# Optimization experiments

Hardware: AMD Instinct MI355X
Metric: run time of the kernel (lower is better)

Reference implementation:

```python
import jax, jax.numpy as jnp
import numpy as np

HIDDEN = 300
INPUT_DIM = 300


def setup_inputs() -> dict:
    key = jax.random.key(0)
    k_in, k_wih, k_whh, k_bih, k_bhh = jax.random.split(key, 5)
    bound = 1.0 / np.sqrt(HIDDEN)  # PyTorch RNNCell init: U(-1/sqrt(H), 1/sqrt(H))
    inputs = jax.random.normal(k_in, (512, 512, INPUT_DIM), dtype=jnp.float32)
    W_ih = jax.random.uniform(k_wih, (HIDDEN, INPUT_DIM), jnp.float32, -bound, bound)
    W_hh = jax.random.uniform(k_whh, (HIDDEN, HIDDEN), jnp.float32, -bound, bound)
    b_ih = jax.random.uniform(k_bih, (HIDDEN,), jnp.float32, -bound, bound)
    b_hh = jax.random.uniform(k_bhh, (HIDDEN,), jnp.float32, -bound, bound)
    return {"inputs": inputs, "W_ih": W_ih, "W_hh": W_hh, "b_ih": b_ih, "b_hh": b_hh}


def reference(inputs, W_ih, W_hh, b_ih, b_hh):
    # inputs: [seq, batch, input_dim]; vanilla tanh RNNCell scanned over time.
    seq, bz, _ = inputs.shape
    # Precompute input projections for all timesteps in one big GEMM.
    x_proj = jnp.einsum('sbi,hi->sbh', inputs, W_ih) + b_ih + b_hh  # [seq, batch, H]

    def step(ht, xp):
        ht = jnp.tanh(xp + ht @ W_hh.T)
        return ht, None

    h0 = jnp.zeros((bz, HIDDEN), dtype=inputs.dtype)
    ht, _ = jax.lax.scan(step, h0, x_proj)
    return ht
```

## Files before the change

### kernel.cpp

```cpp
#include <hip/hip_runtime.h>
#include <hip/hip_bf16.h>


typedef unsigned short u16;
typedef unsigned int   u32;
typedef __attribute__((ext_vector_type(8)))  short bf16x8;
typedef __attribute__((ext_vector_type(4)))  short s16x4;
typedef __attribute__((ext_vector_type(4)))  float f32x4;
typedef __attribute__((ext_vector_type(16))) float f32x16;
typedef __attribute__((ext_vector_type(2)))  unsigned int u32x2;
typedef __attribute__((ext_vector_type(4)))  unsigned int u32x4;

#define HID 300
#define KP  320
#define SEQ 512
#define BZ  512
#define MTOT (SEQ*BZ)

__device__ __forceinline__ u16 f2bf(float f) {
    u32 u = __float_as_uint(f);
    return (u16)((u + 0x7FFFu + ((u >> 16) & 1u)) >> 16);
}
__device__ __forceinline__ float bf2f(u16 h) {
    return __uint_as_float((u32)h << 16);
}
__device__ __forceinline__ float tanh_fast(float x) {
    float e = __builtin_amdgcn_exp2f(x * 2.8853900817779268f);
    float r = __builtin_amdgcn_rcpf(e + 1.0f);
    return __builtin_fmaf(-2.0f, r, 1.0f);
}
__device__ __forceinline__ u32 pack2(float a, float b) {
    __hip_bfloat162 t = __float22bfloat162_rn(float2{a, b});
    return *(u32*)&t;
}
__device__ __forceinline__ void lds_barrier() {
    asm volatile("s_waitcnt lgkmcnt(0)\n\ts_barrier" ::: "memory");
}

__global__ void prep_kernel(const float* __restrict__ wih,
                            const float* __restrict__ whh,
                            const float* __restrict__ bih,
                            const float* __restrict__ bhh,
                            u16* __restrict__ wihp, u16* __restrict__ whhp,
                            float* __restrict__ bias) {
    int n = blockIdx.x, k = threadIdx.x;
    bool v = (n < HID) && (k < HID);
    int src = n * HID + k, dst = n * KP + k;
    wihp[dst] = v ? f2bf(wih[src]) : (u16)0;
    whhp[dst] = v ? f2bf(whh[src]) : (u16)0;
    if (k == 0) bias[n] = (n < HID) ? (bih[n] + bhh[n]) : 0.0f;
}

__global__ __launch_bounds__(512, 1) void xproj_kernel(
    const float* __restrict__ in, const u16* __restrict__ wihp,
    const float* __restrict__ bias, u16* __restrict__ xp) {
    __shared__ __align__(16) u16 As[2][4096];
    __shared__ __align__(16) u16 Bs[2][10240];

    const int tid = threadIdx.x;
    const int w = tid >> 6, l = tid & 63;
    const int mi = w & 3, ni = w >> 2;
    const int l31 = l & 31, l5 = l >> 5;
    const int m0 = blockIdx.x * 128;

    const int sm = tid >> 2, skg = tid & 3;

    f32x16 acc[5];
#pragma unroll
    for (int j = 0; j < 5; ++j)
#pragma unroll
        for (int r = 0; r < 16; ++r) acc[j][r] = 0.0f;

    auto loadA = [&](int it, f32x4& v0, f32x4& v1) {
        int gk = it * 32 + skg * 8;
        const float* p = in + (size_t)(m0 + sm) * HID + gk;
        if (gk <= 292) { v0 = *(const f32x4*)p; v1 = *(const f32x4*)(p + 4); }
        else if (gk <= 296) { v0 = *(const f32x4*)p; v1 = f32x4{0.f,0.f,0.f,0.f}; }
        else { v0 = f32x4{0.f,0.f,0.f,0.f}; v1 = f32x4{0.f,0.f,0.f,0.f}; }
    };
    auto writeA = [&](int buf, const f32x4& v0, const f32x4& v1) {
        u32x4 pk;
        pk[0] = pack2(v0[0], v0[1]); pk[1] = pack2(v0[2], v0[3]);
        pk[2] = pack2(v1[0], v1[1]); pk[3] = pack2(v1[2], v1[3]);
        *(u32x4*)&As[buf][(skg >> 1) * 2048 + sm * 16 + (skg & 1) * 8] = pk;
    };
    auto stageB = [&](int buf, int it) {
#pragma unroll
        for (int s = 0; s < 3; ++s) {
            int i = w + 8 * s;
            if (i < 20) {
                int c = i & 3, ng = i >> 2;
                int n = ng * 64 + l;
                const u16* g = wihp + n * KP + it * 32 + c * 8;
                u16* d = &Bs[buf][c * 2560 + ng * 512];
                __builtin_amdgcn_global_load_lds(
                    (const __attribute__((address_space(1))) void*)g,
                    (__attribute__((address_space(3))) void*)d, 16, 0, 0);
            }
        }
    };

    {
        f32x4 v0, v1;
        loadA(0, v0, v1);
        writeA(0, v0, v1);
        stageB(0, 0);
    }
    __syncthreads();

#pragma unroll 1
    for (int it = 0; it < 10; ++it) {
        const int cb = it & 1, nb = (it + 1) & 1;
        f32x4 v0, v1;
        if (it < 9) {
            loadA(it + 1, v0, v1);
            stageB(nb, it + 1);
        }
#pragma unroll
        for (int s = 0; s < 2; ++s) {
            bf16x8 a = *(const bf16x8*)&As[cb][s * 2048 + mi * 512 + l31 * 16 + l5 * 8];
#pragma unroll
            for (int j = 0; j < 5; ++j) {
                bf16x8 b = *(const bf16x8*)&Bs[cb][(s * 2 + l5) * 2560 + ((ni * 5 + j) * 32 + l31) * 8];
                acc[j] = __builtin_amdgcn_mfma_f32_32x32x16_bf16(a, b, acc[j], 0, 0, 0);
            }
        }
        if (it < 9) writeA(nb, v0, v1);
        __syncthreads();
    }

    const int mbase = m0 + mi * 32;
#pragma unroll
    for (int j = 0; j < 5; ++j) {
        int n = (ni * 5 + j) * 32 + l31;
        if (n < HID) {
            float bs = bias[n];
#pragma unroll
            for (int reg = 0; reg < 16; ++reg) {
                int row = (reg & 3) + 8 * (reg >> 2) + 4 * l5;
                xp[(size_t)(mbase + row) * HID + n] = f2bf(acc[j][reg] + bs);
            }
        }
    }
}

__global__ __launch_bounds__(256, 1) void rnn_recur_kernel(
    const u16* __restrict__ xp, const u16* __restrict__ whhp,
    float* __restrict__ out) {
    __shared__ __align__(16) u16 hb[2][16 * 328];

    const int tid = threadIdx.x;
    const int w = tid >> 6;
    const int l = tid & 63;
    const int br = l & 15;
    const int q  = l >> 4;
    const int b0 = blockIdx.x * 16;

    for (int i = tid; i < (2 * 16 * 328) / 2; i += 256) ((u32*)hb)[i] = 0;

    bf16x8 Af[5][10];
#pragma unroll
    for (int j = 0; j < 5; ++j) {
        const u16* wrow = whhp + (size_t)((w + 4 * j) * 16 + br) * KP;
#pragma unroll
        for (int ks = 0; ks < 10; ++ks)
            Af[j][ks] = *(const bf16x8*)(wrow + ks * 32 + q * 8);
    }
#pragma unroll
    for (int j = 0; j < 5; ++j)
#pragma unroll
        for (int ks = 0; ks < 10; ++ks)
            asm volatile("" : "+a"(Af[j][ks]));

    int xo[5];
#pragma unroll
    for (int j = 0; j < 5; ++j) {
        int n0 = (w + 4 * j) * 16 + q * 4;
        xo[j] = (n0 < HID) ? ((b0 + br) * HID + n0) : -1;
    }

    const s16x4 z4 = {0, 0, 0, 0};
    s16x4 xc[5], xn[5];
#pragma unroll
    for (int j = 0; j < 5; ++j) {
        xc[j] = (xo[j] >= 0) ? *(const s16x4*)(xp + xo[j]) : z4;
        xn[j] = (xo[j] >= 0) ? *(const s16x4*)(xp + (size_t)BZ * HID + xo[j]) : z4;
    }

    lds_barrier();

#pragma unroll 1
    for (int t = 0; t < SEQ; ++t) {
        const u16* hc = hb[t & 1];
        u16*       hn = hb[(t + 1) & 1];

        s16x4 xf[5];
        {
            int t2 = (t + 2 < SEQ) ? (t + 2) : (SEQ - 1);
            const u16* base = xp + (size_t)t2 * (BZ * HID);
#pragma unroll
            for (int j = 0; j < 5; ++j)
                xf[j] = (xo[j] >= 0) ? *(const s16x4*)(base + xo[j]) : z4;
        }

        f32x4 acc[5];
#pragma unroll
        for (int j = 0; j < 5; ++j)
#pragma unroll
            for (int r = 0; r < 4; ++r) acc[j][r] = 0.0f;

#pragma unroll
        for (int ks = 0; ks < 10; ++ks) {
            bf16x8 bfr = *(const bf16x8*)&hc[br * 328 + ks * 32 + q * 8];
#pragma unroll
            for (int j = 0; j < 5; ++j)
                acc[j] = __builtin_amdgcn_mfma_f32_16x16x32_bf16(Af[j][ks], bfr, acc[j], 0, 0, 0);
        }

#pragma unroll
        for (int j = 0; j < 5; ++j) {
            int n0 = (w + 4 * j) * 16 + q * 4;
            float v0 = tanh_fast(acc[j][0] + bf2f((u16)xc[j][0]));
            float v1 = tanh_fast(acc[j][1] + bf2f((u16)xc[j][1]));
            float v2 = tanh_fast(acc[j][2] + bf2f((u16)xc[j][2]));
            float v3 = tanh_fast(acc[j][3] + bf2f((u16)xc[j][3]));
            u32x2 pk;
            pk[0] = pack2(v0, v1);
            pk[1] = pack2(v2, v3);
            *(u32x2*)&hn[br * 328 + n0] = pk;
        }
        lds_barrier();

#pragma unroll
        for (int j = 0; j < 5; ++j) { xc[j] = xn[j]; xn[j] = xf[j]; }
    }

    const u16* hf = hb[0];
    for (int i = tid; i < 16 * HID; i += 256) {
        int r = i / HID, n = i - r * HID;
        out[(size_t)(b0 + r) * HID + n] = bf2f(hf[r * 328 + n]);
    }
}

extern "C" void kernel_launch(void* const* d_in, const int* in_sizes, int n_in,
                              void* d_out, int out_size, void* d_ws, size_t ws_size,
                              hipStream_t stream) {
    const float* in  = (const float*)d_in[0];
    const float* wih = (const float*)d_in[1];
    const float* whh = (const float*)d_in[2];
    const float* bih = (const float*)d_in[3];
    const float* bhh = (const float*)d_in[4];

    char* ws = (char*)d_ws;
    const size_t XP_BYTES = (size_t)MTOT * HID * sizeof(u16);
    u16*   xpb  = (u16*)ws;
    u16*   wihp = (u16*)(ws + XP_BYTES);
    u16*   whhp = (u16*)(ws + XP_BYTES + (size_t)KP * KP * 2);
    float* bias = (float*)(ws + XP_BYTES + 2 * (size_t)KP * KP * 2);

    prep_kernel<<<KP, KP, 0, stream>>>(wih, whh, bih, bhh, wihp, whhp, bias);
    xproj_kernel<<<MTOT / 128, 512, 0, stream>>>(in, wihp, bias, xpb);
    rnn_recur_kernel<<<BZ / 16, 256, 0, stream>>>(xpb, whhp, (float*)d_out);
}
```

Measured before the change: 1.135 ms.

## Spread recurrence N-tiles over eight waves per block instead of four

The recurrent kernel now launches 512 threads (8 waves) per 16-row batch tile. Each wave owns 2 or 3 of the 20 output column tiles instead of 5, which shortens the serial MFMA and tanh chain per timestep. The cost is a barrier across twice as many waves each step, and an uneven split where waves 0-3 carry three tiles and waves 4-7 carry two.

```diff
diff --git a/kernel.cpp b/kernel.cpp
--- a/kernel.cpp
+++ b/kernel.cpp
@@ -144,7 +144,7 @@
     }
 }
 
-__global__ __launch_bounds__(256, 1) void rnn_recur_kernel(
+__global__ __launch_bounds__(512, 2) void rnn_recur_kernel(
     const u16* __restrict__ xp, const u16* __restrict__ whhp,
     float* __restrict__ out) {
     __shared__ __align__(16) u16 hb[2][16 * 328];
@@ -155,34 +155,39 @@
     const int br = l & 15;
     const int q  = l >> 4;
     const int b0 = blockIdx.x * 16;
-
-    for (int i = tid; i < (2 * 16 * 328) / 2; i += 256) ((u32*)hb)[i] = 0;
-
-    bf16x8 Af[5][10];
-#pragma unroll
-    for (int j = 0; j < 5; ++j) {
-        const u16* wrow = whhp + (size_t)((w + 4 * j) * 16 + br) * KP;
-#pragma unroll
-        for (int ks = 0; ks < 10; ++ks)
-            Af[j][ks] = *(const bf16x8*)(wrow + ks * 32 + q * 8);
-    }
-#pragma unroll
-    for (int j = 0; j < 5; ++j)
-#pragma unroll
-        for (int ks = 0; ks < 10; ++ks)
-            asm volatile("" : "+a"(Af[j][ks]));
-
-    int xo[5];
-#pragma unroll
-    for (int j = 0; j < 5; ++j) {
-        int n0 = (w + 4 * j) * 16 + q * 4;
-        xo[j] = (n0 < HID) ? ((b0 + br) * HID + n0) : -1;
+    const bool t3 = (w < 4);
+
+    for (int i = tid; i < (2 * 16 * 328) / 2; i += 512) ((u32*)hb)[i] = 0;
+
+    bf16x8 Af[3][10];
+#pragma unroll
+    for (int j = 0; j < 3; ++j) {
+        if (j < 2 || t3) {
+            const int nt = w + 8 * j;
+            const u16* wrow = whhp + (size_t)(nt * 16 + br) * KP;
+#pragma unroll
+            for (int ks = 0; ks < 10; ++ks)
+                Af[j][ks] = *(const bf16x8*)(wrow + ks * 32 + q * 8);
+        }
+    }
+#pragma unroll
+    for (int j = 0; j < 3; ++j)
+        if (j < 2 || t3)
+#pragma unroll
+            for (int ks = 0; ks < 10; ++ks)
+                asm volatile("" : "+a"(Af[j][ks]));
+
+    int xo[3];
+#pragma unroll
+    for (int j = 0; j < 3; ++j) {
+        int n0 = (w + 8 * j) * 16 + q * 4;
+        xo[j] = (n0 < HID && (j < 2 || t3)) ? ((b0 + br) * HID + n0) : -1;
     }
 
     const s16x4 z4 = {0, 0, 0, 0};
-    s16x4 xc[5], xn[5];
-#pragma unroll
-    for (int j = 0; j < 5; ++j) {
+    s16x4 xc[3], xn[3];
+#pragma unroll
+    for (int j = 0; j < 3; ++j) {
         xc[j] = (xo[j] >= 0) ? *(const s16x4*)(xp + xo[j]) : z4;
         xn[j] = (xo[j] >= 0) ? *(const s16x4*)(xp + (size_t)BZ * HID + xo[j]) : z4;
     }
@@ -194,49 +199,63 @@
         const u16* hc = hb[t & 1];
         u16*       hn = hb[(t + 1) & 1];
 
-        s16x4 xf[5];
+        s16x4 xf[3];
         {
             int t2 = (t + 2 < SEQ) ? (t + 2) : (SEQ - 1);
             const u16* base = xp + (size_t)t2 * (BZ * HID);
 #pragma unroll
-            for (int j = 0; j < 5; ++j)
+            for (int j = 0; j < 3; ++j)
                 xf[j] = (xo[j] >= 0) ? *(const s16x4*)(base + xo[j]) : z4;
         }
 
-        f32x4 acc[5];
-#pragma unroll
-        for (int j = 0; j < 5; ++j)
-#pragma unroll
-            for (int r = 0; r < 4; ++r) acc[j][r] = 0.0f;
+        f32x4 a0, a1, a2;
+#pragma unroll
+        for (int r = 0; r < 4; ++r) { a0[r] = 0.f; a1[r] = 0.f; a2[r] = 0.f; }
 
 #pragma unroll
         for (int ks = 0; ks < 10; ++ks) {
             bf16x8 bfr = *(const bf16x8*)&hc[br * 328 + ks * 32 + q * 8];
-#pragma unroll
-            for (int j = 0; j < 5; ++j)
-                acc[j] = __builtin_amdgcn_mfma_f32_16x16x32_bf16(Af[j][ks], bfr, acc[j], 0, 0, 0);
-        }
-
-#pragma unroll
-        for (int j = 0; j < 5; ++j) {
-            int n0 = (w + 4 * j) * 16 + q * 4;
-            float v0 = tanh_fast(acc[j][0] + bf2f((u16)xc[j][0]));
-            float v1 = tanh_fast(acc[j][1] + bf2f((u16)xc[j][1]));
-            float v2 = tanh_fast(acc[j][2] + bf2f((u16)xc[j][2]));
-            float v3 = tanh_fast(acc[j][3] + bf2f((u16)xc[j][3]));
+            a0 = __builtin_amdgcn_mfma_f32_16x16x32_bf16(Af[0][ks], bfr, a0, 0, 0, 0);
+            a1 = __builtin_amdgcn_mfma_f32_16x16x32_bf16(Af[1][ks], bfr, a1, 0, 0, 0);
+            if (t3)
+                a2 = __builtin_amdgcn_mfma_f32_16x16x32_bf16(Af[2][ks], bfr, a2, 0, 0, 0);
+        }
+
+        {
+            int n0 = w * 16 + q * 4;
             u32x2 pk;
-            pk[0] = pack2(v0, v1);
-            pk[1] = pack2(v2, v3);
+            pk[0] = pack2(tanh_fast(a0[0] + bf2f((u16)xc[0][0])),
+                          tanh_fast(a0[1] + bf2f((u16)xc[0][1])));
+            pk[1] = pack2(tanh_fast(a0[2] + bf2f((u16)xc[0][2])),
+                          tanh_fast(a0[3] + bf2f((u16)xc[0][3])));
             *(u32x2*)&hn[br * 328 + n0] = pk;
         }
+        {
+            int n0 = (w + 8) * 16 + q * 4;
+            u32x2 pk;
+            pk[0] = pack2(tanh_fast(a1[0] + bf2f((u16)xc[1][0])),
+                          tanh_fast(a1[1] + bf2f((u16)xc[1][1])));
+            pk[1] = pack2(tanh_fast(a1[2] + bf2f((u16)xc[1][2])),
+                          tanh_fast(a1[3] + bf2f((u16)xc[1][3])));
+            *(u32x2*)&hn[br * 328 + n0] = pk;
+        }
+        if (t3) {
+            int n0 = (w + 16) * 16 + q * 4;
+            u32x2 pk;
+            pk[0] = pack2(tanh_fast(a2[0] + bf2f((u16)xc[2][0])),
+                          tanh_fast(a2[1] + bf2f((u16)xc[2][1])));
+            pk[1] = pack2(tanh_fast(a2[2] + bf2f((u16)xc[2][2])),
+                          tanh_fast(a2[3] + bf2f((u16)xc[2][3])));
+            *(u32x2*)&hn[br * 328 + n0] = pk;
+        }
         lds_barrier();
 
 #pragma unroll
-        for (int j = 0; j < 5; ++j) { xc[j] = xn[j]; xn[j] = xf[j]; }
+        for (int j = 0; j < 3; ++j) { xc[j] = xn[j]; xn[j] = xf[j]; }
     }
 
     const u16* hf = hb[0];
-    for (int i = tid; i < 16 * HID; i += 256) {
+    for (int i = tid; i < 16 * HID; i += 512) {
         int r = i / HID, n = i - r * HID;
         out[(size_t)(b0 + r) * HID + n] = bf2f(hf[r * 328 + n]);
     }
@@ -260,5 +279,5 @@
 
     prep_kernel<<<KP, KP, 0, stream>>>(wih, whh, bih, bhh, wihp, whhp, bias);
     xproj_kernel<<<MTOT / 128, 512, 0, stream>>>(in, wihp, bias, xpb);
-    rnn_recur_kernel<<<BZ / 16, 256, 0, stream>>>(xpb, whhp, (float*)d_out);
-}
+    rnn_recur_kernel<<<BZ / 16, 512, 0, stream>>>(xpb, whhp, (float*)d_out);
+}
```

Measured after the change: 1.090 ms. -3.9%, faster.
